# Kernel optimization log

Hardware: AMD Instinct MI355X
Metric: run time of the kernel (lower is better)

Reference implementation:

```python
import jax, jax.numpy as jnp
import numpy as np

EPSILON = 1e-8
NUM_STEPS = 1000
S_OFFSET = 0.0001
POWER = 2
CLIPMAX = 0.999
B = 1048576


def _schedule():
    t = jnp.arange(0, NUM_STEPS + 1, dtype=jnp.float32)
    f_t = jnp.cos(np.pi / 2 * (t / NUM_STEPS + S_OFFSET) / (1 + S_OFFSET)) ** POWER
    alpha_bars = f_t / f_t[0]
    betas = jnp.concatenate([jnp.zeros([1], jnp.float32), 1.0 - alpha_bars[1:] / alpha_bars[:-1]])
    betas = jnp.minimum(betas, CLIPMAX)
    sigmas = jnp.sqrt(betas[1:] * ((1.0 - alpha_bars[:-1]) / (1.0 - alpha_bars[1:])))
    sigmas = jnp.concatenate([jnp.zeros([1], jnp.float32), sigmas])
    return alpha_bars, betas, sigmas


def setup_inputs() -> dict:
    key = jax.random.key(0)
    k1, k2, k3, k4, k5 = jax.random.split(key, 5)
    lt = jax.random.normal(k1, (B, 6), dtype=jnp.float32)
    predicted_l0 = jax.random.normal(k2, (B, 6), dtype=jnp.float32)
    pred_lattice = jax.random.normal(k3, (B, 3, 3), dtype=jnp.float32)
    z_noise = jax.random.normal(k4, (B, 6), dtype=jnp.float32)  # torch.randn_like(lt), frozen
    t = jax.random.randint(k5, (B,), 0, NUM_STEPS, dtype=jnp.int64)
    alpha_bars, betas, sigmas = _schedule()
    return {
        "lt": lt,
        "predicted_l0": predicted_l0,
        "pred_lattice": pred_lattice,
        "alpha_bars": alpha_bars,
        "betas": betas,
        "sigmas": sigmas,
        "z_noise": z_noise,
        "t": t,
    }


def reference(lt, predicted_l0, pred_lattice, alpha_bars, betas, sigmas, z_noise, t):
    # VP_lattice.reverse
    alpha = 1.0 - betas[t]
    alpha = jnp.maximum(alpha, 1.0 - betas[-2])  # clamp_min
    alpha_bar = alpha_bars[t]
    sigma = sigmas[t][:, None]

    # polar_decomposition: only the symmetric factor L_tilda = V diag(S) V^T is used
    _, S, Vt = jnp.linalg.svd(pred_lattice, full_matrices=False)  # (B,3),(B,3,3)
    L = jnp.einsum("bji,bj,bjk->bik", Vt, S, Vt)  # Vt^T @ diag(S) @ Vt
    L = (L + jnp.swapaxes(L, 1, 2)) / 2  # symmetrize

    # symmetric_matrix_to_vector: upper triangular incl. diagonal
    vec = jnp.stack([L[:, 0, 0], L[:, 0, 1], L[:, 0, 2], L[:, 1, 1], L[:, 1, 2], L[:, 2, 2]], axis=1)

    predicted_noise = lt - (vec + predicted_l0) / 2
    z = jnp.where((t > 1)[:, None], z_noise, jnp.zeros_like(z_noise))
    coef = (1.0 / jnp.sqrt(alpha + EPSILON))[:, None]
    scale = ((1.0 - alpha) / jnp.sqrt(1.0 - alpha_bar + EPSILON))[:, None]
    return coef * (lt - scale * predicted_noise) + sigma * z
```

## Files before the change

### kernel.cpp

```cpp
#include <hip/hip_runtime.h>


#define NUM_STEPS 1000

__global__ __launch_bounds__(256) void vp_lattice_kernel(
    const float* __restrict__ lt,
    const float* __restrict__ pl0,
    const float* __restrict__ plat,
    const float* __restrict__ alpha_bars,
    const float* __restrict__ betas,
    const float* __restrict__ sigmas,
    const float* __restrict__ z_noise,
    const int*   __restrict__ t,
    float* __restrict__ out,
    int n)
{
    __shared__ float sCoef[NUM_STEPS + 1];
    __shared__ float sScale[NUM_STEPS + 1];
    __shared__ float sSig[NUM_STEPS + 1];
    {
        float beta_last = betas[NUM_STEPS - 1];
        for (int j = threadIdx.x; j <= NUM_STEPS; j += 256) {
            float alpha = 1.0f - fminf(betas[j], beta_last);
            sCoef[j]  = 1.0f / sqrtf(alpha + 1e-8f);
            sScale[j] = (1.0f - alpha) / sqrtf(1.0f - alpha_bars[j] + 1e-8f);
            sSig[j]   = (j > 1) ? sigmas[j] : 0.0f;
        }
    }
    __syncthreads();

    int i = blockIdx.x * blockDim.x + threadIdx.x;
    if (i >= n) return;

    size_t b9 = (size_t)i * 9;
    float a00 = plat[b9+0], a01 = plat[b9+1], a02 = plat[b9+2];
    float a10 = plat[b9+3], a11 = plat[b9+4], a12 = plat[b9+5];
    float a20 = plat[b9+6], a21 = plat[b9+7], a22 = plat[b9+8];

    float m00 = a00*a00 + a10*a10 + a20*a20;
    float m01 = a00*a01 + a10*a11 + a20*a21;
    float m02 = a00*a02 + a10*a12 + a20*a22;
    float m11 = a01*a01 + a11*a11 + a21*a21;
    float m12 = a01*a02 + a11*a12 + a21*a22;
    float m22 = a02*a02 + a12*a12 + a22*a22;

    float q  = (m00 + m11 + m22) * (1.0f/3.0f);
    float b00 = m00 - q, b11 = m11 - q, b22 = m22 - q;
    float p1 = m01*m01 + m02*m02 + m12*m12;
    float p2 = b00*b00 + b11*b11 + b22*b22 + 2.0f*p1;
    float p  = sqrtf(p2 * (1.0f/6.0f));
    float detB = b00*(b11*b22 - m12*m12)
               - m01*(m01*b22 - m12*m02)
               + m02*(m01*m12 - b11*m02);
    float pinv = 1.0f / fmaxf(p, 1e-20f);
    float r = 0.5f * detB * pinv * pinv * pinv;
    r = fminf(fmaxf(r, -1.0f), 1.0f);
    float phi = acosf(r) * (1.0f/3.0f);
    float mu1 = q + 2.0f*p*cosf(phi);
    float mu3 = q + 2.0f*p*cosf(phi + 2.0943951023931953f);
    float mu2 = 3.0f*q - mu1 - mu3;
    float l1 = sqrtf(fmaxf(mu1, 0.0f));
    float l2 = sqrtf(fmaxf(mu2, 0.0f));
    float l3 = sqrtf(fmaxf(mu3, 0.0f));

    float IU   = l1 + l2 + l3;
    float IIU  = l1*(l2 + l3) + l2*l3;
    float IIIU = l1*l2*l3;
    float denom = (l1 + l2) * (l1 + l3) * (l2 + l3);
    float dinv  = 1.0f / fmaxf(denom, 1e-25f);
    float sd = (IU*IU - IIU) * dinv;
    float td = IU * IIIU * dinv;
    float nd = -dinv;

    float mm00 = m00*m00 + m01*m01 + m02*m02;
    float mm01 = m00*m01 + m01*m11 + m02*m12;
    float mm02 = m00*m02 + m01*m12 + m02*m22;
    float mm11 = m01*m01 + m11*m11 + m12*m12;
    float mm12 = m01*m02 + m11*m12 + m12*m22;
    float mm22 = m02*m02 + m12*m12 + m22*m22;

    float v0 = nd*mm00 + sd*m00 + td;
    float v1 = nd*mm01 + sd*m01;
    float v2 = nd*mm02 + sd*m02;
    float v3 = nd*mm11 + sd*m11 + td;
    float v4 = nd*mm12 + sd*m12;
    float v5 = nd*mm22 + sd*m22 + td;

    int ti = t[i];
    float coef  = sCoef[ti];
    float scale = sScale[ti];
    float sig   = sSig[ti];

    size_t b6 = (size_t)i * 6;
    const float2* lt2 = reinterpret_cast<const float2*>(lt + b6);
    const float2* p02 = reinterpret_cast<const float2*>(pl0 + b6);
    const float2* zn2 = reinterpret_cast<const float2*>(z_noise + b6);
    float2* out2      = reinterpret_cast<float2*>(out + b6);

    float lv[6], pv[6], zv[6];
    float2 w;
    w = lt2[0]; lv[0]=w.x; lv[1]=w.y;
    w = lt2[1]; lv[2]=w.x; lv[3]=w.y;
    w = lt2[2]; lv[4]=w.x; lv[5]=w.y;
    w = p02[0]; pv[0]=w.x; pv[1]=w.y;
    w = p02[1]; pv[2]=w.x; pv[3]=w.y;
    w = p02[2]; pv[4]=w.x; pv[5]=w.y;
    w = zn2[0]; zv[0]=w.x; zv[1]=w.y;
    w = zn2[1]; zv[2]=w.x; zv[3]=w.y;
    w = zn2[2]; zv[4]=w.x; zv[5]=w.y;

    float vv[6] = {v0, v1, v2, v3, v4, v5};
    float ov[6];
#pragma unroll
    for (int c = 0; c < 6; ++c) {
        float lc = lv[c];
        float pn = lc - 0.5f * (vv[c] + pv[c]);
        ov[c] = coef * (lc - scale * pn) + sig * zv[c];
    }
    out2[0] = make_float2(ov[0], ov[1]);
    out2[1] = make_float2(ov[2], ov[3]);
    out2[2] = make_float2(ov[4], ov[5]);
}

extern "C" void kernel_launch(void* const* d_in, const int* in_sizes, int n_in,
                              void* d_out, int out_size, void* d_ws, size_t ws_size,
                              hipStream_t stream) {
    const float* lt         = (const float*)d_in[0];
    const float* pl0        = (const float*)d_in[1];
    const float* plat       = (const float*)d_in[2];
    const float* alpha_bars = (const float*)d_in[3];
    const float* betas      = (const float*)d_in[4];
    const float* sigmas     = (const float*)d_in[5];
    const float* z_noise    = (const float*)d_in[6];
    const int*   t          = (const int*)d_in[7];
    float* out = (float*)d_out;

    int n = in_sizes[0] / 6;
    int block = 256;
    int grid = (n + block - 1) / block;
    vp_lattice_kernel<<<grid, block, 0, stream>>>(
        lt, pl0, plat, alpha_bars, betas, sigmas, z_noise, t, out, n);
}
```

Baseline: 153.6 us.

## Stage lattice and per-row results through LDS for coalesced float4 global access

The 3x3 lattice block for each workgroup is now loaded cooperatively with coalesced float4 reads into shared memory, and each thread reads its own matrix from there. The six-element outputs and per-row coefficients are written back to shared memory, so the elementwise phase can read lt, predicted_l0 and z_noise and write out as contiguous float4 chunks instead of strided float2 accesses. The aim is better memory coalescing on a bandwidth-bound kernel. The cost is extra barriers, more LDS use that may lower occupancy, and a 9-float LDS stride that can cause bank conflicts.

```diff
diff --git a/kernel.cpp b/kernel.cpp
--- a/kernel.cpp
+++ b/kernel.cpp
@@ -15,27 +15,45 @@
     float* __restrict__ out,
     int n)
 {
-    __shared__ float sCoef[NUM_STEPS + 1];
-    __shared__ float sScale[NUM_STEPS + 1];
-    __shared__ float sSig[NUM_STEPS + 1];
+    __shared__ float sTabCoef[NUM_STEPS + 1];
+    __shared__ float sTabScale[NUM_STEPS + 1];
+    __shared__ float sTabSig[NUM_STEPS + 1];
+    __shared__ __align__(16) float sReg[2304];
+
+    const int tid = threadIdx.x;
+    const int bid = blockIdx.x;
+
     {
         float beta_last = betas[NUM_STEPS - 1];
-        for (int j = threadIdx.x; j <= NUM_STEPS; j += 256) {
+        for (int j = tid; j <= NUM_STEPS; j += 256) {
             float alpha = 1.0f - fminf(betas[j], beta_last);
-            sCoef[j]  = 1.0f / sqrtf(alpha + 1e-8f);
-            sScale[j] = (1.0f - alpha) / sqrtf(1.0f - alpha_bars[j] + 1e-8f);
-            sSig[j]   = (j > 1) ? sigmas[j] : 0.0f;
+            sTabCoef[j]  = 1.0f / sqrtf(alpha + 1e-8f);
+            sTabScale[j] = (1.0f - alpha) / sqrtf(1.0f - alpha_bars[j] + 1e-8f);
+            sTabSig[j]   = (j > 1) ? sigmas[j] : 0.0f;
         }
     }
+
+    {
+        const float4* plat4 = reinterpret_cast<const float4*>(plat);
+        const size_t pb = (size_t)bid * 576;
+        const size_t pmax = (size_t)n * 9 / 4;
+        float4* s4 = reinterpret_cast<float4*>(sReg);
+#pragma unroll
+        for (int j = 0; j < 3; ++j) {
+            int k = tid + j * 256;
+            if (k < 576 && pb + k < pmax) s4[k] = plat4[pb + k];
+        }
+    }
+
+    const int row = bid * 256 + tid;
+    int ti = (row < n) ? t[row] : 0;
+
     __syncthreads();
 
-    int i = blockIdx.x * blockDim.x + threadIdx.x;
-    if (i >= n) return;
-
-    size_t b9 = (size_t)i * 9;
-    float a00 = plat[b9+0], a01 = plat[b9+1], a02 = plat[b9+2];
-    float a10 = plat[b9+3], a11 = plat[b9+4], a12 = plat[b9+5];
-    float a20 = plat[b9+6], a21 = plat[b9+7], a22 = plat[b9+8];
+    const float* A = sReg + tid * 9;
+    float a00 = A[0], a01 = A[1], a02 = A[2];
+    float a10 = A[3], a11 = A[4], a12 = A[5];
+    float a20 = A[6], a21 = A[7], a22 = A[8];
 
     float m00 = a00*a00 + a10*a10 + a20*a20;
     float m01 = a00*a01 + a10*a11 + a20*a21;
@@ -86,40 +104,65 @@
     float v4 = nd*mm12 + sd*m12;
     float v5 = nd*mm22 + sd*m22 + td;
 
-    int ti = t[i];
-    float coef  = sCoef[ti];
-    float scale = sScale[ti];
-    float sig   = sSig[ti];
+    float coefR  = sTabCoef[ti];
+    float scaleR = sTabScale[ti];
+    float sigR   = sTabSig[ti];
 
-    size_t b6 = (size_t)i * 6;
-    const float2* lt2 = reinterpret_cast<const float2*>(lt + b6);
-    const float2* p02 = reinterpret_cast<const float2*>(pl0 + b6);
-    const float2* zn2 = reinterpret_cast<const float2*>(z_noise + b6);
-    float2* out2      = reinterpret_cast<float2*>(out + b6);
+    __syncthreads();
 
-    float lv[6], pv[6], zv[6];
-    float2 w;
-    w = lt2[0]; lv[0]=w.x; lv[1]=w.y;
-    w = lt2[1]; lv[2]=w.x; lv[3]=w.y;
-    w = lt2[2]; lv[4]=w.x; lv[5]=w.y;
-    w = p02[0]; pv[0]=w.x; pv[1]=w.y;
-    w = p02[1]; pv[2]=w.x; pv[3]=w.y;
-    w = p02[2]; pv[4]=w.x; pv[5]=w.y;
-    w = zn2[0]; zv[0]=w.x; zv[1]=w.y;
-    w = zn2[1]; zv[2]=w.x; zv[3]=w.y;
-    w = zn2[2]; zv[4]=w.x; zv[5]=w.y;
+    float* sVec   = sReg;
+    float* sCoef  = sReg + 1536;
+    float* sScale = sReg + 1792;
+    float* sSig   = sReg + 2048;
+    {
+        float* v = sVec + tid * 6;
+        v[0] = v0; v[1] = v1; v[2] = v2; v[3] = v3; v[4] = v4; v[5] = v5;
+        sCoef[tid] = coefR; sScale[tid] = scaleR; sSig[tid] = sigR;
+    }
+    __syncthreads();
 
-    float vv[6] = {v0, v1, v2, v3, v4, v5};
-    float ov[6];
+    const float4* lt4 = reinterpret_cast<const float4*>(lt);
+    const float4* pl4 = reinterpret_cast<const float4*>(pl0);
+    const float4* zn4 = reinterpret_cast<const float4*>(z_noise);
+    float4* out4      = reinterpret_cast<float4*>(out);
+    const size_t cbase  = (size_t)bid * 384;
+    const size_t cmax   = (size_t)n * 6 / 4;
+
 #pragma unroll
-    for (int c = 0; c < 6; ++c) {
-        float lc = lv[c];
-        float pn = lc - 0.5f * (vv[c] + pv[c]);
-        ov[c] = coef * (lc - scale * pn) + sig * zv[c];
+    for (int pass = 0; pass < 2; ++pass) {
+        int lc = tid + pass * 256;
+        if (lc >= 384) break;
+        size_t qg = cbase + lc;
+        if (lc < 384 && qg < cmax) {
+            int lf = lc * 4;
+            float4 l4 = lt4[qg];
+            float4 p4 = pl4[qg];
+            float4 z4 = zn4[qg];
+            float4 vf = *reinterpret_cast<const float4*>(sVec + lf);
+
+            int r0 = lf / 6;
+            int c0 = lf - r0 * 6;
+            int r1 = (lf + 3) / 6;
+            float cf0 = sCoef[r0], sc0 = sScale[r0], sg0 = sSig[r0];
+            float cf1 = sCoef[r1], sc1 = sScale[r1], sg1 = sSig[r1];
+
+            float lv[4] = {l4.x, l4.y, l4.z, l4.w};
+            float pv[4] = {p4.x, p4.y, p4.z, p4.w};
+            float zv[4] = {z4.x, z4.y, z4.z, z4.w};
+            float vv[4] = {vf.x, vf.y, vf.z, vf.w};
+            float ov[4];
+#pragma unroll
+            for (int e = 0; e < 4; ++e) {
+                bool second = (c0 + e) >= 6;
+                float cf = second ? cf1 : cf0;
+                float sc = second ? sc1 : sc0;
+                float sg = second ? sg1 : sg0;
+                float pn = lv[e] - 0.5f * (vv[e] + pv[e]);
+                ov[e] = cf * (lv[e] - sc * pn) + sg * zv[e];
+            }
+            out4[qg] = make_float4(ov[0], ov[1], ov[2], ov[3]);
+        }
     }
-    out2[0] = make_float2(ov[0], ov[1]);
-    out2[1] = make_float2(ov[2], ov[3]);
-    out2[2] = make_float2(ov[4], ov[5]);
 }
 
 extern "C" void kernel_launch(void* const* d_in, const int* in_sizes, int n_in,
@@ -136,8 +179,7 @@
     float* out = (float*)d_out;
 
     int n = in_sizes[0] / 6;
-    int block = 256;
-    int grid = (n + block - 1) / block;
-    vp_lattice_kernel<<<grid, block, 0, stream>>>(
+    int grid = (n + 255) / 256;
+    vp_lattice_kernel<<<grid, 256, 0, stream>>>(
         lt, pl0, plat, alpha_bars, betas, sigmas, z_noise, t, out, n);
 }
```

Result: slower. 161.8 us (+5.3%).

## Process four rows per thread with 128-bit nontemporal loads and stores

Applied to the files above, without the earlier changes.

Each thread now handles four consecutive batch rows, so all input and output arrays can be read and written as aligned float4 vectors using nontemporal hints. The global loads are issued before the shared-memory barrier so they overlap the table setup. This raises per-thread register pressure and cuts the grid to a quarter of the threads. It also silently drops any tail rows when n is not a multiple of four.

```diff
diff --git a/kernel.cpp b/kernel.cpp
--- a/kernel.cpp
+++ b/kernel.cpp
@@ -2,6 +2,9 @@
 
 
 #define NUM_STEPS 1000
+
+typedef float  f4 __attribute__((ext_vector_type(4)));
+typedef int    i4 __attribute__((ext_vector_type(4)));
 
 __global__ __launch_bounds__(256) void vp_lattice_kernel(
     const float* __restrict__ lt,
@@ -13,7 +16,7 @@
     const float* __restrict__ z_noise,
     const int*   __restrict__ t,
     float* __restrict__ out,
-    int n)
+    int nquad)
 {
     __shared__ float sCoef[NUM_STEPS + 1];
     __shared__ float sScale[NUM_STEPS + 1];
@@ -27,99 +30,110 @@
             sSig[j]   = (j > 1) ? sigmas[j] : 0.0f;
         }
     }
+
+    int gid = blockIdx.x * blockDim.x + threadIdx.x;
+    if (gid >= nquad) { __syncthreads(); return; }
+
+    const f4* plat4 = reinterpret_cast<const f4*>(plat)    + (size_t)gid * 9;
+    const f4* lt4   = reinterpret_cast<const f4*>(lt)      + (size_t)gid * 6;
+    const f4* pl4   = reinterpret_cast<const f4*>(pl0)     + (size_t)gid * 6;
+    const f4* zn4   = reinterpret_cast<const f4*>(z_noise) + (size_t)gid * 6;
+    i4 tt = reinterpret_cast<const i4*>(t)[gid];
+
+    f4 A4[9], L4[6], P4[6], Z4[6];
+#pragma unroll
+    for (int j = 0; j < 9; ++j) A4[j] = __builtin_nontemporal_load(&plat4[j]);
+#pragma unroll
+    for (int j = 0; j < 6; ++j) L4[j] = __builtin_nontemporal_load(&lt4[j]);
+#pragma unroll
+    for (int j = 0; j < 6; ++j) P4[j] = __builtin_nontemporal_load(&pl4[j]);
+#pragma unroll
+    for (int j = 0; j < 6; ++j) Z4[j] = __builtin_nontemporal_load(&zn4[j]);
+
+    const float* Af = reinterpret_cast<const float*>(A4);
+    const float* Lf = reinterpret_cast<const float*>(L4);
+    const float* Pf = reinterpret_cast<const float*>(P4);
+    const float* Zf = reinterpret_cast<const float*>(Z4);
+    int tis[4] = {tt.x, tt.y, tt.z, tt.w};
+
     __syncthreads();
 
-    int i = blockIdx.x * blockDim.x + threadIdx.x;
-    if (i >= n) return;
+    float ov[24];
+#pragma unroll
+    for (int r = 0; r < 4; ++r) {
+        const float* A = Af + r * 9;
+        float a00 = A[0], a01 = A[1], a02 = A[2];
+        float a10 = A[3], a11 = A[4], a12 = A[5];
+        float a20 = A[6], a21 = A[7], a22 = A[8];
 
-    size_t b9 = (size_t)i * 9;
-    float a00 = plat[b9+0], a01 = plat[b9+1], a02 = plat[b9+2];
-    float a10 = plat[b9+3], a11 = plat[b9+4], a12 = plat[b9+5];
-    float a20 = plat[b9+6], a21 = plat[b9+7], a22 = plat[b9+8];
+        float m00 = a00*a00 + a10*a10 + a20*a20;
+        float m01 = a00*a01 + a10*a11 + a20*a21;
+        float m02 = a00*a02 + a10*a12 + a20*a22;
+        float m11 = a01*a01 + a11*a11 + a21*a21;
+        float m12 = a01*a02 + a11*a12 + a21*a22;
+        float m22 = a02*a02 + a12*a12 + a22*a22;
 
-    float m00 = a00*a00 + a10*a10 + a20*a20;
-    float m01 = a00*a01 + a10*a11 + a20*a21;
-    float m02 = a00*a02 + a10*a12 + a20*a22;
-    float m11 = a01*a01 + a11*a11 + a21*a21;
-    float m12 = a01*a02 + a11*a12 + a21*a22;
-    float m22 = a02*a02 + a12*a12 + a22*a22;
+        float q  = (m00 + m11 + m22) * (1.0f/3.0f);
+        float b00 = m00 - q, b11 = m11 - q, b22 = m22 - q;
+        float p1 = m01*m01 + m02*m02 + m12*m12;
+        float p2 = b00*b00 + b11*b11 + b22*b22 + 2.0f*p1;
+        float p  = sqrtf(p2 * (1.0f/6.0f));
+        float detB = b00*(b11*b22 - m12*m12)
+                   - m01*(m01*b22 - m12*m02)
+                   + m02*(m01*m12 - b11*m02);
+        float pinv = 1.0f / fmaxf(p, 1e-20f);
+        float rr = 0.5f * detB * pinv * pinv * pinv;
+        rr = fminf(fmaxf(rr, -1.0f), 1.0f);
+        float phi = acosf(rr) * (1.0f/3.0f);
+        float mu1 = q + 2.0f*p*cosf(phi);
+        float mu3 = q + 2.0f*p*cosf(phi + 2.0943951023931953f);
+        float mu2 = 3.0f*q - mu1 - mu3;
+        float l1 = sqrtf(fmaxf(mu1, 0.0f));
+        float l2 = sqrtf(fmaxf(mu2, 0.0f));
+        float l3 = sqrtf(fmaxf(mu3, 0.0f));
 
-    float q  = (m00 + m11 + m22) * (1.0f/3.0f);
-    float b00 = m00 - q, b11 = m11 - q, b22 = m22 - q;
-    float p1 = m01*m01 + m02*m02 + m12*m12;
-    float p2 = b00*b00 + b11*b11 + b22*b22 + 2.0f*p1;
-    float p  = sqrtf(p2 * (1.0f/6.0f));
-    float detB = b00*(b11*b22 - m12*m12)
-               - m01*(m01*b22 - m12*m02)
-               + m02*(m01*m12 - b11*m02);
-    float pinv = 1.0f / fmaxf(p, 1e-20f);
-    float r = 0.5f * detB * pinv * pinv * pinv;
-    r = fminf(fmaxf(r, -1.0f), 1.0f);
-    float phi = acosf(r) * (1.0f/3.0f);
-    float mu1 = q + 2.0f*p*cosf(phi);
-    float mu3 = q + 2.0f*p*cosf(phi + 2.0943951023931953f);
-    float mu2 = 3.0f*q - mu1 - mu3;
-    float l1 = sqrtf(fmaxf(mu1, 0.0f));
-    float l2 = sqrtf(fmaxf(mu2, 0.0f));
-    float l3 = sqrtf(fmaxf(mu3, 0.0f));
+        float IU   = l1 + l2 + l3;
+        float IIU  = l1*(l2 + l3) + l2*l3;
+        float IIIU = l1*l2*l3;
+        float denom = (l1 + l2) * (l1 + l3) * (l2 + l3);
+        float dinv  = 1.0f / fmaxf(denom, 1e-25f);
+        float sd = (IU*IU - IIU) * dinv;
+        float td = IU * IIIU * dinv;
+        float nd = -dinv;
 
-    float IU   = l1 + l2 + l3;
-    float IIU  = l1*(l2 + l3) + l2*l3;
-    float IIIU = l1*l2*l3;
-    float denom = (l1 + l2) * (l1 + l3) * (l2 + l3);
-    float dinv  = 1.0f / fmaxf(denom, 1e-25f);
-    float sd = (IU*IU - IIU) * dinv;
-    float td = IU * IIIU * dinv;
-    float nd = -dinv;
+        float mm00 = m00*m00 + m01*m01 + m02*m02;
+        float mm01 = m00*m01 + m01*m11 + m02*m12;
+        float mm02 = m00*m02 + m01*m12 + m02*m22;
+        float mm11 = m01*m01 + m11*m11 + m12*m12;
+        float mm12 = m01*m02 + m11*m12 + m12*m22;
+        float mm22 = m02*m02 + m12*m12 + m22*m22;
 
-    float mm00 = m00*m00 + m01*m01 + m02*m02;
-    float mm01 = m00*m01 + m01*m11 + m02*m12;
-    float mm02 = m00*m02 + m01*m12 + m02*m22;
-    float mm11 = m01*m01 + m11*m11 + m12*m12;
-    float mm12 = m01*m02 + m11*m12 + m12*m22;
-    float mm22 = m02*m02 + m12*m12 + m22*m22;
+        float vv[6];
+        vv[0] = nd*mm00 + sd*m00 + td;
+        vv[1] = nd*mm01 + sd*m01;
+        vv[2] = nd*mm02 + sd*m02;
+        vv[3] = nd*mm11 + sd*m11 + td;
+        vv[4] = nd*mm12 + sd*m12;
+        vv[5] = nd*mm22 + sd*m22 + td;
 
-    float v0 = nd*mm00 + sd*m00 + td;
-    float v1 = nd*mm01 + sd*m01;
-    float v2 = nd*mm02 + sd*m02;
-    float v3 = nd*mm11 + sd*m11 + td;
-    float v4 = nd*mm12 + sd*m12;
-    float v5 = nd*mm22 + sd*m22 + td;
+        int ti = tis[r];
+        float coef  = sCoef[ti];
+        float scale = sScale[ti];
+        float sig   = sSig[ti];
+#pragma unroll
+        for (int c = 0; c < 6; ++c) {
+            float lc = Lf[r*6 + c];
+            float pn = lc - 0.5f * (vv[c] + Pf[r*6 + c]);
+            ov[r*6 + c] = coef * (lc - scale * pn) + sig * Zf[r*6 + c];
+        }
+    }
 
-    int ti = t[i];
-    float coef  = sCoef[ti];
-    float scale = sScale[ti];
-    float sig   = sSig[ti];
-
-    size_t b6 = (size_t)i * 6;
-    const float2* lt2 = reinterpret_cast<const float2*>(lt + b6);
-    const float2* p02 = reinterpret_cast<const float2*>(pl0 + b6);
-    const float2* zn2 = reinterpret_cast<const float2*>(z_noise + b6);
-    float2* out2      = reinterpret_cast<float2*>(out + b6);
-
-    float lv[6], pv[6], zv[6];
-    float2 w;
-    w = lt2[0]; lv[0]=w.x; lv[1]=w.y;
-    w = lt2[1]; lv[2]=w.x; lv[3]=w.y;
-    w = lt2[2]; lv[4]=w.x; lv[5]=w.y;
-    w = p02[0]; pv[0]=w.x; pv[1]=w.y;
-    w = p02[1]; pv[2]=w.x; pv[3]=w.y;
-    w = p02[2]; pv[4]=w.x; pv[5]=w.y;
-    w = zn2[0]; zv[0]=w.x; zv[1]=w.y;
-    w = zn2[1]; zv[2]=w.x; zv[3]=w.y;
-    w = zn2[2]; zv[4]=w.x; zv[5]=w.y;
-
-    float vv[6] = {v0, v1, v2, v3, v4, v5};
-    float ov[6];
+    f4* out4 = reinterpret_cast<f4*>(out) + (size_t)gid * 6;
 #pragma unroll
-    for (int c = 0; c < 6; ++c) {
-        float lc = lv[c];
-        float pn = lc - 0.5f * (vv[c] + pv[c]);
-        ov[c] = coef * (lc - scale * pn) + sig * zv[c];
+    for (int j = 0; j < 6; ++j) {
+        f4 o = {ov[4*j], ov[4*j+1], ov[4*j+2], ov[4*j+3]};
+        __builtin_nontemporal_store(o, &out4[j]);
     }
-    out2[0] = make_float2(ov[0], ov[1]);
-    out2[1] = make_float2(ov[2], ov[3]);
-    out2[2] = make_float2(ov[4], ov[5]);
 }
 
 extern "C" void kernel_launch(void* const* d_in, const int* in_sizes, int n_in,
@@ -136,8 +150,9 @@
     float* out = (float*)d_out;
 
     int n = in_sizes[0] / 6;
+    int nquad = n / 4;
     int block = 256;
-    int grid = (n + block - 1) / block;
+    int grid = (nquad + block - 1) / block;
     vp_lattice_kernel<<<grid, block, 0, stream>>>(
-        lt, pl0, plat, alpha_bars, betas, sigmas, z_noise, t, out, n);
+        lt, pl0, plat, alpha_bars, betas, sigmas, z_noise, t, out, nquad);
 }
```

After: 186.3 us. 21.3% more time.
